# Kernel tuning notes

Measured on AMD Instinct MI355X. Metric: run time of the kernel, lower is better.

The kernel has to match this reference:

```python
import jax, jax.numpy as jnp
import numpy as np

EMB = 128
B = 1024          # number of graphs (segments)
N = 500000        # total nodes
NEG_SLOPE = 0.01  # torch LeakyReLU default


def leaky_relu(v):
    return jnp.where(v >= 0, v, NEG_SLOPE * v)


def setup_inputs() -> dict:
    key = jax.random.key(0)
    ks = jax.random.split(key, 9)
    xg_old = jax.random.normal(ks[0], (B, EMB), dtype=jnp.float32)
    x = jax.random.normal(ks[1], (N, EMB), dtype=jnp.float32)
    batch = jnp.sort(jax.random.randint(ks[2], (N,), 0, B)).astype(jnp.int64)
    s = 1.0 / np.sqrt(EMB)
    w_mask = jax.random.uniform(ks[3], (EMB, 1), jnp.float32, -s, s)
    b_mask = jax.random.uniform(ks[4], (1,), jnp.float32, -s, s)
    w_feat = jax.random.uniform(ks[5], (EMB, EMB), jnp.float32, -s, s)
    b_feat = jax.random.uniform(ks[6], (EMB,), jnp.float32, -s, s)
    s2 = 1.0 / np.sqrt(2 * EMB)
    w_tr = jax.random.uniform(ks[7], (2 * EMB, EMB), jnp.float32, -s2, s2)
    b_tr = jax.random.uniform(ks[8], (EMB,), jnp.float32, -s2, s2)
    return {"xg_old": xg_old, "x": x, "batch": batch,
            "w_mask": w_mask, "b_mask": b_mask,
            "w_feat": w_feat, "b_feat": b_feat,
            "w_tr": w_tr, "b_tr": b_tr}


def reference(xg_old, x, batch, w_mask, b_mask, w_feat, b_feat, w_tr, b_tr):
    batch = batch.astype(jnp.int32)
    # gate score per node, segment-stable softmax over each graph
    gate = (x @ w_mask + b_mask)[:, 0]                        # [N]
    m = jax.ops.segment_max(gate, batch, num_segments=B)      # [B]
    e = jnp.exp(gate - m[batch])                              # [N]
    denom = jax.ops.segment_sum(e, batch, num_segments=B)     # [B]
    alpha = e / denom[batch]                                  # [N]
    # transformed node features, weighted segment-sum pooling
    feat = leaky_relu(x @ w_feat + b_feat)                    # [N, EMB]
    xg = jax.ops.segment_sum(alpha[:, None] * feat, batch, num_segments=B)  # [B, EMB]
    # concat with old global state, linear + LeakyReLU, residual
    cat = jnp.concatenate([xg, xg_old], axis=1)               # [B, 2*EMB]
    out = leaky_relu(cat @ w_tr + b_tr) + xg_old              # [B, EMB]
    return out
```

## Files before the change

kernel.cpp:

```cpp
#include <hip/hip_runtime.h>

typedef __attribute__((ext_vector_type(8))) short short8;
typedef __attribute__((ext_vector_type(4))) float floatx4;

__device__ __forceinline__ float b2f(unsigned int u) { return __uint_as_float(u << 16); }
__device__ __forceinline__ unsigned short f2b(float f) {
    unsigned int u = __float_as_uint(f);
    return (unsigned short)((u + 0x7fffu + ((u >> 16) & 1u)) >> 16);
}

#define EMB 128
#define NN  500000
#define BB  1024
#define BM  128
#define NCT 9

__global__ void kdetect(const unsigned short* __restrict__ xr,
                        const int* __restrict__ braw, int* __restrict__ flags, int N)
{
    int lane = threadIdx.x;
    int good = 0;
#pragma unroll
    for (int j = 0; j < 4; ++j) {
        unsigned short u = xr[lane * 4 + j];
        unsigned e = (u >> 7) & 0xffu;
        if ((e >= 100u && e <= 140u) || u == 0) ++good;
    }
#pragma unroll
    for (int o = 1; o < 64; o <<= 1) good += __shfl_xor(good, o);
    if (lane == 0) {
        flags[0] = (good < 240) ? 1 : 0;
        flags[1] = (braw[N - 1] == 0 && braw[N - 2] != 0) ? 1 : 0;
    }
}

__global__ __launch_bounds__(256)
void kinit(float* __restrict__ denom, float* __restrict__ xg,
           unsigned short* __restrict__ wTf, const void* __restrict__ w_feat_,
           const void* __restrict__ w_mask_, const int* __restrict__ flags)
{
    int i = blockIdx.x * 256 + threadIdx.x;
    if (i < BB) denom[i] = 0.f;
    if (i < BB * EMB) xg[i] = 0.f;
    if (i < 4 * NCT * 512) {
        int blk = i >> 9, rem = i & 511;
        int lane = rem >> 3, j = rem & 7;
        int kk = blk / NCT, ct = blk - kk * NCT;
        int n = ct * 16 + (lane & 15);
        int k = kk * 32 + (lane >> 4) * 8 + j;
        unsigned short v = 0;
        if (n < 128)      v = flags[0] ? f2b(((const float*)w_feat_)[k * EMB + n])
                                       : ((const unsigned short*)w_feat_)[k * EMB + n];
        else if (n == 128) v = flags[0] ? f2b(((const float*)w_mask_)[k])
                                        : ((const unsigned short*)w_mask_)[k];
        wTf[i] = v;
    }
}

__global__ __launch_bounds__(256, 3)
void kmain(const void* __restrict__ x_, const int* __restrict__ braw,
           const void* __restrict__ bm_, const void* __restrict__ bf_,
           const unsigned short* __restrict__ wTf, const int* __restrict__ flags,
           float* __restrict__ denom, float* __restrict__ xg, int N)
{
    __shared__ float se[BM];
    __shared__ int   sb[BM];

    int tid = threadIdx.x;
    int wave = tid >> 6, lane = tid & 63;
    int quad = lane >> 4, l16 = lane & 15;
    int woff = wave * 32;
    int n0 = blockIdx.x * BM + woff;
    bool f32  = flags[0] != 0;
    bool is64 = flags[1] != 0;

    if (lane < 32) {
        int n = n0 + lane; int s = -1;
        if (n < N) { int v = is64 ? braw[2 * n] : braw[n]; if (v >= 0 && v < BB) s = v; }
        sb[woff + lane] = s;
    }

    short8 afr[2][4];
    if (f32) {
        const float* xf = (const float*)x_;
        float4 av[16];
        float4 z = make_float4(0.f, 0.f, 0.f, 0.f);
#pragma unroll
        for (int i = 0; i < 16; ++i) av[i] = z;
#pragma unroll
        for (int rt = 0; rt < 2; ++rt) {
            int n = n0 + rt * 16 + l16;
            const float* p = xf + (size_t)n * EMB + quad * 8;
            if (n < N) {
#pragma unroll
                for (int kk = 0; kk < 4; ++kk) {
                    av[rt * 8 + kk * 2]     = *(const float4*)(p + kk * 32);
                    av[rt * 8 + kk * 2 + 1] = *(const float4*)(p + kk * 32 + 4);
                }
            }
        }
#pragma unroll
        for (int rt = 0; rt < 2; ++rt)
#pragma unroll
            for (int kk = 0; kk < 4; ++kk) {
                float4 a = av[rt * 8 + kk * 2], b = av[rt * 8 + kk * 2 + 1];
                short8 t;
                t[0] = (short)f2b(a.x); t[1] = (short)f2b(a.y);
                t[2] = (short)f2b(a.z); t[3] = (short)f2b(a.w);
                t[4] = (short)f2b(b.x); t[5] = (short)f2b(b.y);
                t[6] = (short)f2b(b.z); t[7] = (short)f2b(b.w);
                afr[rt][kk] = t;
            }
    } else {
        const unsigned short* xu = (const unsigned short*)x_;
        short8 z8 = {0, 0, 0, 0, 0, 0, 0, 0};
#pragma unroll
        for (int rt = 0; rt < 2; ++rt) {
            int n = n0 + rt * 16 + l16;
            const unsigned short* p = xu + (size_t)n * EMB + quad * 8;
#pragma unroll
            for (int kk = 0; kk < 4; ++kk) afr[rt][kk] = z8;
            if (n < N) {
#pragma unroll
                for (int kk = 0; kk < 4; ++kk)
                    afr[rt][kk] = *(const short8*)(p + kk * 32);
            }
        }
    }

    floatx4 zero = {0.f, 0.f, 0.f, 0.f};
    floatx4 acc[2][NCT];
#pragma unroll
    for (int rt = 0; rt < 2; ++rt)
#pragma unroll
        for (int ct = 0; ct < NCT; ++ct) acc[rt][ct] = zero;

#pragma unroll
    for (int kk = 0; kk < 4; ++kk) {
#pragma unroll
        for (int ct = 0; ct < NCT; ++ct) {
            short8 bf = *(const short8*)(wTf + ((kk * NCT + ct) << 9) + (lane << 3));
            acc[0][ct] = __builtin_amdgcn_mfma_f32_16x16x32_bf16(afr[0][kk], bf, acc[0][ct], 0, 0, 0);
            acc[1][ct] = __builtin_amdgcn_mfma_f32_16x16x32_bf16(afr[1][kk], bf, acc[1][ct], 0, 0, 0);
        }
    }

    if (l16 == 0) {
#pragma unroll
        for (int rt = 0; rt < 2; ++rt)
#pragma unroll
            for (int r = 0; r < 4; ++r)
                se[woff + rt * 16 + quad * 4 + r] = acc[rt][8][r];
    }

    float bm = f32 ? ((const float*)bm_)[0]
                   : b2f((unsigned int)((const unsigned short*)bm_)[0]);

    if (lane < 32) {
        int sv = sb[woff + lane];
        float g = se[woff + lane] + bm;
        float ev = (sv >= 0) ? __expf(fminf(g, 60.f)) : 0.f;
        se[woff + lane] = ev;
        float v = ev;
#pragma unroll
        for (int o = 1; o < 32; o <<= 1) {
            float u  = __shfl_up(v, o);
            int   su = __shfl_up(sv, o);
            if (lane >= o && su == sv) v += u;
        }
        int sn = __shfl_down(sv, 1);
        if (sv >= 0 && (lane == 31 || sn != sv)) atomicAdd(&denom[sv], v);
    }

    float bfv[8];
#pragma unroll
    for (int ct = 0; ct < 8; ++ct)
        bfv[ct] = f32 ? ((const float*)bf_)[ct * 16 + l16]
                      : b2f((unsigned int)((const unsigned short*)bf_)[ct * 16 + l16]);

    float er[2][4]; int sr[2][4];
#pragma unroll
    for (int rt = 0; rt < 2; ++rt)
#pragma unroll
        for (int r = 0; r < 4; ++r) {
            int lr = rt * 16 + quad * 4 + r;
            er[rt][r] = se[woff + lr];
            sr[rt][r] = sb[woff + lr];
        }

    int sF = sb[woff], sL = sb[woff + 31];
    if (sF == sL) {
        if (sF >= 0) {
#pragma unroll
            for (int ct = 0; ct < 8; ++ct) {
                float p = 0.f;
#pragma unroll
                for (int rt = 0; rt < 2; ++rt)
#pragma unroll
                    for (int r = 0; r < 4; ++r) {
                        float v = acc[rt][ct][r] + bfv[ct];
                        v = v >= 0.f ? v : 0.01f * v;
                        p += v * er[rt][r];
                    }
                p += __shfl_xor(p, 16);
                p += __shfl_xor(p, 32);
                if (quad == (ct & 3))
                    atomicAdd(&xg[sF * EMB + ct * 16 + l16], p);
            }
        }
    } else {
#pragma unroll
        for (int ct = 0; ct < 8; ++ct) {
            int col = ct * 16 + l16;
#pragma unroll
            for (int rt = 0; rt < 2; ++rt) {
                float a = 0.f; int cur = -1;
#pragma unroll
                for (int r = 0; r < 4; ++r) {
                    int s = sr[rt][r];
                    float v = acc[rt][ct][r] + bfv[ct];
                    v = v >= 0.f ? v : 0.01f * v;
                    v *= er[rt][r];
                    if (s != cur) {
                        if (cur >= 0) atomicAdd(&xg[cur * EMB + col], a);
                        a = 0.f; cur = s;
                    }
                    if (s >= 0) a += v;
                }
                if (cur >= 0) atomicAdd(&xg[cur * EMB + col], a);
            }
        }
    }
}

__global__ __launch_bounds__(128)
void kfinal(const float* __restrict__ xg, const float* __restrict__ denom,
            const void* __restrict__ xg_old_, const void* __restrict__ w_tr_,
            const void* __restrict__ b_tr_, const int* __restrict__ flags,
            void* __restrict__ out_)
{
    __shared__ float cat[2 * EMB];
    int b = blockIdx.x, j = threadIdx.x;
    bool f32 = flags[0] != 0;

    float d = denom[b];
    float xgv = xg[b * EMB + j];
    xgv = (d > 0.f) ? xgv / d : 0.f;
    if (xgv != xgv) xgv = 700.0f;
    cat[j] = xgv;
    float old = f32 ? ((const float*)xg_old_)[b * EMB + j]
                    : b2f((unsigned int)((const unsigned short*)xg_old_)[b * EMB + j]);
    cat[EMB + j] = old;
    __syncthreads();

    float acc = f32 ? ((const float*)b_tr_)[j]
                    : b2f((unsigned int)((const unsigned short*)b_tr_)[j]);
    if (f32) {
        const float* w = (const float*)w_tr_;
#pragma unroll 8
        for (int i = 0; i < 2 * EMB; ++i) acc = fmaf(cat[i], w[i * EMB + j], acc);
    } else {
        const unsigned short* w = (const unsigned short*)w_tr_;
#pragma unroll 8
        for (int i = 0; i < 2 * EMB; ++i) acc = fmaf(cat[i], b2f((unsigned int)w[i * EMB + j]), acc);
    }
    acc = acc >= 0.f ? acc : 0.01f * acc;
    acc += old;
    if (acc != acc) acc = 300.0f;

    if (f32) ((float*)out_)[b * EMB + j] = acc;
    else     ((unsigned short*)out_)[b * EMB + j] = f2b(acc);
}

extern "C" void kernel_launch(void* const* d_in, const int* in_sizes, int n_in,
                              void* d_out, int out_size, void* d_ws, size_t ws_size,
                              hipStream_t stream) {
    const void* xg_old = d_in[0];
    const void* x      = d_in[1];
    const int*  braw   = (const int*)d_in[2];
    const void* w_mask = d_in[3];
    const void* b_mask = d_in[4];
    const void* w_feat = d_in[5];
    const void* b_feat = d_in[6];
    const void* w_tr   = d_in[7];
    const void* b_tr   = d_in[8];

    const int N = NN;

    char* ws = (char*)d_ws;
    size_t off = 0;
    int*   flags = (int*)(ws + off);   off += 64;
    float* denom = (float*)(ws + off); off += (size_t)BB * 4;
    float* xg    = (float*)(ws + off); off += (size_t)BB * EMB * 4;
    unsigned short* wTf = (unsigned short*)(ws + off); off += (size_t)4 * NCT * 512 * 2;

    kdetect<<<1, 64, 0, stream>>>((const unsigned short*)x, braw, flags, N);
    kinit<<<(BB * EMB + 255) / 256, 256, 0, stream>>>(denom, xg, wTf, w_feat, w_mask, flags);
    kmain<<<(N + BM - 1) / BM, 256, 0, stream>>>(x, braw, b_mask, b_feat, wTf,
                                                 flags, denom, xg, N);
    kfinal<<<BB, 128, 0, stream>>>(xg, denom, xg_old, w_tr, b_tr, flags, d_out);
}
```

Before: 404.5 us.

## Make main kernel persistent with double-buffered tile loads and per-segment register accumulation

Replaces the one-block-per-128-nodes launch with a fixed grid of 512 blocks. Each wave walks a contiguous range of 32-node tiles and prefetches the next tile's x rows into registers while computing the current one. Pooled features are accumulated in registers across tiles that share a segment, and atomics are issued only when the segment changes, which cuts global atomic traffic. The f32-to-bf16 conversion now uses the packed v_cvt_pk_bf16_f32 instruction. The trade-offs are higher register pressure (launch bounds occupancy hint drops from 3 to 2), a tail imbalance when the tile count does not divide evenly, and less latency hiding from having many resident blocks.

```diff
diff --git a/kernel.cpp b/kernel.cpp
--- a/kernel.cpp
+++ b/kernel.cpp
@@ -8,12 +8,17 @@
     unsigned int u = __float_as_uint(f);
     return (unsigned short)((u + 0x7fffu + ((u >> 16) & 1u)) >> 16);
 }
+__device__ __forceinline__ unsigned cvtpk(float lo, float hi) {
+    unsigned r;
+    asm("v_cvt_pk_bf16_f32 %0, %1, %2" : "=v"(r) : "v"(lo), "v"(hi));
+    return r;
+}
 
 #define EMB 128
 #define NN  500000
 #define BB  1024
-#define BM  128
 #define NCT 9
+#define GRID 512
 
 __global__ void kdetect(const unsigned short* __restrict__ xr,
                         const int* __restrict__ braw, int* __restrict__ flags, int N)
@@ -57,75 +62,38 @@
     }
 }
 
-__global__ __launch_bounds__(256, 3)
-void kmain(const void* __restrict__ x_, const int* __restrict__ braw,
-           const void* __restrict__ bm_, const void* __restrict__ bf_,
-           const unsigned short* __restrict__ wTf, const int* __restrict__ flags,
-           float* __restrict__ denom, float* __restrict__ xg, int N)
-{
-    __shared__ float se[BM];
-    __shared__ int   sb[BM];
-
-    int tid = threadIdx.x;
-    int wave = tid >> 6, lane = tid & 63;
-    int quad = lane >> 4, l16 = lane & 15;
-    int woff = wave * 32;
-    int n0 = blockIdx.x * BM + woff;
-    bool f32  = flags[0] != 0;
-    bool is64 = flags[1] != 0;
+__device__ __forceinline__ void flush_racc(float (&racc)[8], int& runSeg,
+                                           int quad, int l16, float* __restrict__ xg)
+{
+    if (runSeg >= 0) {
+#pragma unroll
+        for (int ct = 0; ct < 8; ++ct) {
+            float p = racc[ct];
+            p += __shfl_xor(p, 16);
+            p += __shfl_xor(p, 32);
+            if (quad == (ct & 3))
+                atomicAdd(&xg[runSeg * EMB + ct * 16 + l16], p);
+            racc[ct] = 0.f;
+        }
+    }
+    runSeg = -1;
+}
+
+__device__ __forceinline__ void tile_compute(
+    const short8 (&afr)[2][4], int t, int N, bool is64,
+    const int* __restrict__ braw, const unsigned short* __restrict__ wTf,
+    float bm, const float (&bfv)[8],
+    float* __restrict__ se, int* __restrict__ sb, int woff,
+    int lane, int quad, int l16,
+    float* __restrict__ denom, float* __restrict__ xg,
+    float (&racc)[8], int& runSeg)
+{
+    int nb = t << 5;
 
     if (lane < 32) {
-        int n = n0 + lane; int s = -1;
+        int n = nb + lane; int s = -1;
         if (n < N) { int v = is64 ? braw[2 * n] : braw[n]; if (v >= 0 && v < BB) s = v; }
         sb[woff + lane] = s;
-    }
-
-    short8 afr[2][4];
-    if (f32) {
-        const float* xf = (const float*)x_;
-        float4 av[16];
-        float4 z = make_float4(0.f, 0.f, 0.f, 0.f);
-#pragma unroll
-        for (int i = 0; i < 16; ++i) av[i] = z;
-#pragma unroll
-        for (int rt = 0; rt < 2; ++rt) {
-            int n = n0 + rt * 16 + l16;
-            const float* p = xf + (size_t)n * EMB + quad * 8;
-            if (n < N) {
-#pragma unroll
-                for (int kk = 0; kk < 4; ++kk) {
-                    av[rt * 8 + kk * 2]     = *(const float4*)(p + kk * 32);
-                    av[rt * 8 + kk * 2 + 1] = *(const float4*)(p + kk * 32 + 4);
-                }
-            }
-        }
-#pragma unroll
-        for (int rt = 0; rt < 2; ++rt)
-#pragma unroll
-            for (int kk = 0; kk < 4; ++kk) {
-                float4 a = av[rt * 8 + kk * 2], b = av[rt * 8 + kk * 2 + 1];
-                short8 t;
-                t[0] = (short)f2b(a.x); t[1] = (short)f2b(a.y);
-                t[2] = (short)f2b(a.z); t[3] = (short)f2b(a.w);
-                t[4] = (short)f2b(b.x); t[5] = (short)f2b(b.y);
-                t[6] = (short)f2b(b.z); t[7] = (short)f2b(b.w);
-                afr[rt][kk] = t;
-            }
-    } else {
-        const unsigned short* xu = (const unsigned short*)x_;
-        short8 z8 = {0, 0, 0, 0, 0, 0, 0, 0};
-#pragma unroll
-        for (int rt = 0; rt < 2; ++rt) {
-            int n = n0 + rt * 16 + l16;
-            const unsigned short* p = xu + (size_t)n * EMB + quad * 8;
-#pragma unroll
-            for (int kk = 0; kk < 4; ++kk) afr[rt][kk] = z8;
-            if (n < N) {
-#pragma unroll
-                for (int kk = 0; kk < 4; ++kk)
-                    afr[rt][kk] = *(const short8*)(p + kk * 32);
-            }
-        }
     }
 
     floatx4 zero = {0.f, 0.f, 0.f, 0.f};
@@ -152,9 +120,6 @@
             for (int r = 0; r < 4; ++r)
                 se[woff + rt * 16 + quad * 4 + r] = acc[rt][8][r];
     }
-
-    float bm = f32 ? ((const float*)bm_)[0]
-                   : b2f((unsigned int)((const unsigned short*)bm_)[0]);
 
     if (lane < 32) {
         int sv = sb[woff + lane];
@@ -172,25 +137,17 @@
         if (sv >= 0 && (lane == 31 || sn != sv)) atomicAdd(&denom[sv], v);
     }
 
-    float bfv[8];
-#pragma unroll
-    for (int ct = 0; ct < 8; ++ct)
-        bfv[ct] = f32 ? ((const float*)bf_)[ct * 16 + l16]
-                      : b2f((unsigned int)((const unsigned short*)bf_)[ct * 16 + l16]);
-
-    float er[2][4]; int sr[2][4];
+    float er[2][4];
 #pragma unroll
     for (int rt = 0; rt < 2; ++rt)
 #pragma unroll
-        for (int r = 0; r < 4; ++r) {
-            int lr = rt * 16 + quad * 4 + r;
-            er[rt][r] = se[woff + lr];
-            sr[rt][r] = sb[woff + lr];
-        }
+        for (int r = 0; r < 4; ++r)
+            er[rt][r] = se[woff + rt * 16 + quad * 4 + r];
 
     int sF = sb[woff], sL = sb[woff + 31];
     if (sF == sL) {
         if (sF >= 0) {
+            if (sF != runSeg) { flush_racc(racc, runSeg, quad, l16, xg); runSeg = sF; }
 #pragma unroll
             for (int ct = 0; ct < 8; ++ct) {
                 float p = 0.f;
@@ -202,13 +159,17 @@
                         v = v >= 0.f ? v : 0.01f * v;
                         p += v * er[rt][r];
                     }
-                p += __shfl_xor(p, 16);
-                p += __shfl_xor(p, 32);
-                if (quad == (ct & 3))
-                    atomicAdd(&xg[sF * EMB + ct * 16 + l16], p);
+                racc[ct] += p;
             }
         }
     } else {
+        flush_racc(racc, runSeg, quad, l16, xg);
+        int sr[2][4];
+#pragma unroll
+        for (int rt = 0; rt < 2; ++rt)
+#pragma unroll
+            for (int r = 0; r < 4; ++r)
+                sr[rt][r] = sb[woff + rt * 16 + quad * 4 + r];
 #pragma unroll
         for (int ct = 0; ct < 8; ++ct) {
             int col = ct * 16 + l16;
@@ -233,6 +194,148 @@
     }
 }
 
+__global__ __launch_bounds__(256, 2)
+void kmain(const void* __restrict__ x_, const int* __restrict__ braw,
+           const void* __restrict__ bm_, const void* __restrict__ bf_,
+           const unsigned short* __restrict__ wTf, const int* __restrict__ flags,
+           float* __restrict__ denom, float* __restrict__ xg, int N)
+{
+    __shared__ float se[128];
+    __shared__ int   sb[128];
+
+    int tid = threadIdx.x;
+    int wave = tid >> 6, lane = tid & 63;
+    int quad = lane >> 4, l16 = lane & 15;
+    int woff = wave * 32;
+    bool f32  = flags[0] != 0;
+    bool is64 = flags[1] != 0;
+
+    int T  = (N + 31) >> 5;
+    int NW = gridDim.x * 4;
+    int C  = (T + NW - 1) / NW;
+    int W  = blockIdx.x * 4 + wave;
+    int t0 = W * C;
+    int tend = t0 + C; if (tend > T) tend = T;
+    if (t0 >= tend) return;
+
+    float bm = f32 ? ((const float*)bm_)[0]
+                   : b2f((unsigned int)((const unsigned short*)bm_)[0]);
+    float bfv[8];
+#pragma unroll
+    for (int ct = 0; ct < 8; ++ct)
+        bfv[ct] = f32 ? ((const float*)bf_)[ct * 16 + l16]
+                      : b2f((unsigned int)((const unsigned short*)bf_)[ct * 16 + l16]);
+
+    float racc[8];
+#pragma unroll
+    for (int ct = 0; ct < 8; ++ct) racc[ct] = 0.f;
+    int runSeg = -1;
+
+    if (f32) {
+        const float* xf = (const float*)x_;
+        float4 rA[16], rB[16];
+        float4 fz = make_float4(0.f, 0.f, 0.f, 0.f);
+
+#define LOADF(dst, tt) do {                                                     \
+        int nb_ = (tt) << 5;                                                    \
+        _Pragma("unroll")                                                       \
+        for (int rt = 0; rt < 2; ++rt) {                                        \
+            int n_ = nb_ + rt * 16 + l16;                                       \
+            const float* p_ = xf + (size_t)n_ * EMB + quad * 8;                 \
+            _Pragma("unroll")                                                   \
+            for (int kk = 0; kk < 4; ++kk) {                                    \
+                dst[rt * 8 + kk * 2]     = (n_ < N) ? *(const float4*)(p_ + kk * 32)     : fz; \
+                dst[rt * 8 + kk * 2 + 1] = (n_ < N) ? *(const float4*)(p_ + kk * 32 + 4) : fz; \
+            }                                                                   \
+        }                                                                       \
+    } while (0)
+
+#define CONVF(afr, src) do {                                                    \
+        _Pragma("unroll")                                                       \
+        for (int rt = 0; rt < 2; ++rt)                                          \
+            _Pragma("unroll")                                                   \
+            for (int kk = 0; kk < 4; ++kk) {                                    \
+                float4 a_ = src[rt * 8 + kk * 2], b_ = src[rt * 8 + kk * 2 + 1];\
+                union { short8 s; unsigned u[4]; } cv_;                         \
+                cv_.u[0] = cvtpk(a_.x, a_.y); cv_.u[1] = cvtpk(a_.z, a_.w);     \
+                cv_.u[2] = cvtpk(b_.x, b_.y); cv_.u[3] = cvtpk(b_.z, b_.w);     \
+                afr[rt][kk] = cv_.s;                                            \
+            }                                                                   \
+    } while (0)
+
+        int t = t0;
+        LOADF(rA, t);
+        while (true) {
+            {
+                short8 afr[2][4];
+                CONVF(afr, rA);
+                if (t + 1 < tend) LOADF(rB, t + 1);
+                tile_compute(afr, t, N, is64, braw, wTf, bm, bfv,
+                             se, sb, woff, lane, quad, l16, denom, xg, racc, runSeg);
+                ++t; if (t >= tend) break;
+            }
+            {
+                short8 afr[2][4];
+                CONVF(afr, rB);
+                if (t + 1 < tend) LOADF(rA, t + 1);
+                tile_compute(afr, t, N, is64, braw, wTf, bm, bfv,
+                             se, sb, woff, lane, quad, l16, denom, xg, racc, runSeg);
+                ++t; if (t >= tend) break;
+            }
+        }
+#undef LOADF
+#undef CONVF
+    } else {
+        const unsigned short* xu = (const unsigned short*)x_;
+        short8 hA[8], hB[8];
+        short8 hz = {0, 0, 0, 0, 0, 0, 0, 0};
+
+#define LOADH(dst, tt) do {                                                     \
+        int nb_ = (tt) << 5;                                                    \
+        _Pragma("unroll")                                                       \
+        for (int rt = 0; rt < 2; ++rt) {                                        \
+            int n_ = nb_ + rt * 16 + l16;                                       \
+            const unsigned short* p_ = xu + (size_t)n_ * EMB + quad * 8;        \
+            _Pragma("unroll")                                                   \
+            for (int kk = 0; kk < 4; ++kk)                                      \
+                dst[rt * 4 + kk] = (n_ < N) ? *(const short8*)(p_ + kk * 32) : hz; \
+        }                                                                       \
+    } while (0)
+
+#define COPYH(afr, src) do {                                                    \
+        _Pragma("unroll")                                                       \
+        for (int rt = 0; rt < 2; ++rt)                                          \
+            _Pragma("unroll")                                                   \
+            for (int kk = 0; kk < 4; ++kk) afr[rt][kk] = src[rt * 4 + kk];      \
+    } while (0)
+
+        int t = t0;
+        LOADH(hA, t);
+        while (true) {
+            {
+                short8 afr[2][4];
+                COPYH(afr, hA);
+                if (t + 1 < tend) LOADH(hB, t + 1);
+                tile_compute(afr, t, N, is64, braw, wTf, bm, bfv,
+                             se, sb, woff, lane, quad, l16, denom, xg, racc, runSeg);
+                ++t; if (t >= tend) break;
+            }
+            {
+                short8 afr[2][4];
+                COPYH(afr, hB);
+                if (t + 1 < tend) LOADH(hA, t + 1);
+                tile_compute(afr, t, N, is64, braw, wTf, bm, bfv,
+                             se, sb, woff, lane, quad, l16, denom, xg, racc, runSeg);
+                ++t; if (t >= tend) break;
+            }
+        }
+#undef LOADH
+#undef COPYH
+    }
+
+    flush_racc(racc, runSeg, quad, l16, xg);
+}
+
 __global__ __launch_bounds__(128)
 void kfinal(const float* __restrict__ xg, const float* __restrict__ denom,
             const void* __restrict__ xg_old_, const void* __restrict__ w_tr_,
@@ -296,7 +399,6 @@
 
     kdetect<<<1, 64, 0, stream>>>((const unsigned short*)x, braw, flags, N);
     kinit<<<(BB * EMB + 255) / 256, 256, 0, stream>>>(denom, xg, wTf, w_feat, w_mask, flags);
-    kmain<<<(N + BM - 1) / BM, 256, 0, stream>>>(x, braw, b_mask, b_feat, wTf,
-                                                 flags, denom, xg, N);
+    kmain<<<GRID, 256, 0, stream>>>(x, braw, b_mask, b_feat, wTf, flags, denom, xg, N);
     kfinal<<<BB, 128, 0, stream>>>(xg, denom, xg_old, w_tr, b_tr, flags, d_out);
 }
```

Result: slower. 641.0 us (+58.5%).
